# Optimization experiments

Measured on AMD Instinct MI355X. Metric: run time of the kernel, lower is better.

## Reference

```python
import jax, jax.numpy as jnp
import numpy as np

N, E, G = 50000, 800000, 512
F_IN, ED, NUM_CLASSES = 128, 3, 10
H1, C1, C2 = 4, 32, 64


def _add_self_loops(src, dst, eattr, n):
    # PyG add_self_loops with fill_value='mean': loop attr = mean of incoming edge attrs
    cnt = jax.ops.segment_sum(jnp.ones_like(dst, dtype=eattr.dtype), dst, num_segments=n)
    loop = jax.ops.segment_sum(eattr, dst, num_segments=n) / jnp.maximum(cnt, 1.0)[:, None]
    ar = jnp.arange(n)
    return (jnp.concatenate([src, ar]), jnp.concatenate([dst, ar]),
            jnp.concatenate([eattr, loop], axis=0))


def _gatv2(x, src, dst, eattr, Wl, bl, Wr, br, We, att, bias, heads, out_ch, concat, n):
    xl = (x @ Wl.T + bl).reshape(n, heads, out_ch)   # source transform (lin_l)
    xr = (x @ Wr.T + br).reshape(n, heads, out_ch)   # target transform (lin_r)
    ee = (eattr @ We.T).reshape(-1, heads, out_ch)   # edge transform (lin_edge, no bias)
    m = jax.nn.leaky_relu(xl[src] + xr[dst] + ee, 0.2)  # [E', H, C]
    score = jnp.einsum('ehc,hc->eh', m, att)
    # segment softmax over incoming edges of each target node
    smax = jax.ops.segment_max(score, dst, num_segments=n)
    ex = jnp.exp(score - smax[dst])
    denom = jax.ops.segment_sum(ex, dst, num_segments=n)
    alpha = ex / denom[dst]
    out = jax.ops.segment_sum(alpha[:, :, None] * xl[src], dst, num_segments=n)
    out = out.reshape(n, heads * out_ch) if concat else out.mean(axis=1)
    return out + bias


def setup_inputs() -> dict:
    key = jax.random.key(0)
    ks = jax.random.split(key, 24)
    s = 0.1
    return {
        'x': jax.random.normal(ks[0], (N, F_IN), jnp.float32),
        'edge_index': jax.random.randint(ks[1], (2, E), 0, N),
        'edge_attr': jax.random.normal(ks[2], (E, ED), jnp.float32),
        'batch': jnp.sort(jax.random.randint(ks[3], (N,), 0, G)),
        'u': jax.random.normal(ks[4], (G, 1), jnp.float32),
        'Wl1': jax.random.normal(ks[5], (H1 * C1, F_IN), jnp.float32) * s,
        'bl1': jnp.zeros((H1 * C1,), jnp.float32),
        'Wr1': jax.random.normal(ks[6], (H1 * C1, F_IN), jnp.float32) * s,
        'br1': jnp.zeros((H1 * C1,), jnp.float32),
        'We1': jax.random.normal(ks[7], (H1 * C1, ED), jnp.float32) * s,
        'att1': jax.random.normal(ks[8], (H1, C1), jnp.float32) * s,
        'b1': jnp.zeros((H1 * C1,), jnp.float32),
        'Wl2': jax.random.normal(ks[9], (C2, H1 * C1), jnp.float32) * s,
        'bl2': jnp.zeros((C2,), jnp.float32),
        'Wr2': jax.random.normal(ks[10], (C2, H1 * C1), jnp.float32) * s,
        'br2': jnp.zeros((C2,), jnp.float32),
        'We2': jax.random.normal(ks[11], (C2, ED), jnp.float32) * s,
        'att2': jax.random.normal(ks[12], (1, C2), jnp.float32) * s,
        'b2': jnp.zeros((C2,), jnp.float32),
        'W_lin1': jax.random.normal(ks[13], (32, 65), jnp.float32) * s,
        'b_lin1': jnp.zeros((32,), jnp.float32),
        'W_head': jax.random.normal(ks[14], (NUM_CLASSES, 32), jnp.float32) * s,
        'b_head': jnp.zeros((NUM_CLASSES,), jnp.float32),
    }


def reference(x, edge_index, edge_attr, batch, u,
              Wl1, bl1, Wr1, br1, We1, att1, b1,
              Wl2, bl2, Wr2, br2, We2, att2, b2,
              W_lin1, b_lin1, W_head, b_head):
    n = x.shape[0]
    src, dst, ea = _add_self_loops(edge_index[0], edge_index[1], edge_attr, n)
    h = jax.nn.elu(_gatv2(x, src, dst, ea, Wl1, bl1, Wr1, br1, We1, att1, b1, H1, C1, True, n))
    h = jax.nn.elu(_gatv2(h, src, dst, ea, Wl2, bl2, Wr2, br2, We2, att2, b2, 1, C2, False, n))
    cnt = jax.ops.segment_sum(jnp.ones((n,), h.dtype), batch, num_segments=G)
    pooled = jax.ops.segment_sum(h, batch, num_segments=G) / jnp.maximum(cnt, 1.0)[:, None]
    z = jax.nn.relu(jnp.concatenate([pooled, u], axis=1) @ W_lin1.T + b_lin1)
    return z @ W_head.T + b_head
```

## Files before the change

kernel.cpp:

```cpp
#include <hip/hip_runtime.h>
#include <hip/hip_fp16.h>
#include <math.h>


union H2U { __half2 h; unsigned u; };
typedef _Float16 hv2_t __attribute__((ext_vector_type(2)));
typedef unsigned uv4_t __attribute__((ext_vector_type(4)));
typedef _Float16 f16x8 __attribute__((ext_vector_type(8)));
typedef float f32x4 __attribute__((ext_vector_type(4)));

__device__ __forceinline__ __half2 hmax2(__half2 a, __half2 b) {
  union { __half2 h; hv2_t v; } x, y, r;
  x.h = a; y.h = b;
  r.v = __builtin_elementwise_max(x.v, y.v);
  return r.h;
}

#if __has_builtin(__builtin_amdgcn_fdot2)
__device__ __forceinline__ float dot2f(__half2 a, __half2 b, float c) {
  union { __half2 h; hv2_t v; } x, y;
  x.h = a; y.h = b;
  return __builtin_amdgcn_fdot2(x.v, y.v, c, false);
}
#else
__device__ __forceinline__ float dot2f(__half2 a, __half2 b, float c) {
  float2 af = __half22float2(a), bf = __half22float2(b);
  return fmaf(af.x, bf.x, fmaf(af.y, bf.y, c));
}
#endif

#if __has_builtin(__builtin_amdgcn_exp2f)
__device__ __forceinline__ float fexp2(float x) { return __builtin_amdgcn_exp2f(x); }
#else
__device__ __forceinline__ float fexp2(float x) { return exp2f(x); }
#endif

#if __has_builtin(__builtin_amdgcn_update_dpp)
template <int CTRL>
__device__ __forceinline__ float dpp_add(float v) {
  int r = __builtin_amdgcn_update_dpp(0, __builtin_bit_cast(int, v),
                                      CTRL, 0xf, 0xf, true);
  return v + __builtin_bit_cast(float, r);
}
__device__ __forceinline__ float row_sum16(float v) {
  v = dpp_add<0x121>(v);
  v = dpp_add<0x122>(v);
  v = dpp_add<0x124>(v);
  v = dpp_add<0x128>(v);
  return v;
}
#else
__device__ __forceinline__ float row_sum16(float v) {
  v += __shfl_xor(v, 1);
  v += __shfl_xor(v, 2);
  v += __shfl_xor(v, 4);
  v += __shfl_xor(v, 8);
  return v;
}
#endif

__device__ __forceinline__ float lowf(unsigned u) {
  H2U t; t.u = u;
  return __half2float(__low2half(t.h));
}

__device__ __forceinline__ float eluf(float x) {
  return x > 0.f ? x : __expf(x) - 1.0f;
}

__device__ __forceinline__ f16x8 cvt8(const float* __restrict__ p) {
  float4 v0 = *(const float4*)p;
  float4 v1 = *(const float4*)(p + 4);
  H2U h0, h1, h2, h3;
  h0.h = __floats2half2_rn(v0.x, v0.y);
  h1.h = __floats2half2_rn(v0.z, v0.w);
  h2.h = __floats2half2_rn(v1.x, v1.y);
  h3.h = __floats2half2_rn(v1.z, v1.w);
  union { uv4_t u; f16x8 v; } r;
  r.u = (uv4_t){h0.u, h1.u, h2.u, h3.u};
  return r.v;
}

#define LOG2E 1.44269504088896f

__global__ void hist_k(const int* __restrict__ dst, int* __restrict__ deg,
                       int* __restrict__ rank, int E) {
  int e = blockIdx.x * 256 + threadIdx.x;
  if (e < E) rank[e] = atomicAdd(&deg[dst[e]], 1);
}

__global__ void blocksum_k(const int* __restrict__ deg, int* __restrict__ bsum, int N) {
  __shared__ int s[256];
  int i = blockIdx.x * 256 + threadIdx.x;
  s[threadIdx.x] = (i < N) ? deg[i] : 0;
  __syncthreads();
  for (int off = 128; off; off >>= 1) {
    if (threadIdx.x < off) s[threadIdx.x] += s[threadIdx.x + off];
    __syncthreads();
  }
  if (threadIdx.x == 0) bsum[blockIdx.x] = s[0];
}

__global__ void writeptr_k(const int* __restrict__ deg, const int* __restrict__ bsum,
                           int* __restrict__ rowptr, int N, int E) {
  __shared__ int s[256];
  __shared__ int bs[256];
  int t = threadIdx.x;
  int i = blockIdx.x * 256 + t;
  bs[t] = (t < (int)blockIdx.x) ? bsum[t] : 0;
  s[t] = (i < N) ? deg[i] : 0;
  __syncthreads();
  for (int off = 128; off; off >>= 1) {
    if (t < off) bs[t] += bs[t + off];
    __syncthreads();
  }
  int base = bs[0];
  __syncthreads();
  for (int off = 1; off < 256; off <<= 1) {
    int v = (t >= off) ? s[t - off] : 0;
    __syncthreads();
    if (t >= off) s[t] += v;
    __syncthreads();
  }
  int excl = base + ((t == 0) ? 0 : s[t - 1]) + i;
  if (i < N) rowptr[i] = excl;
  if (i == N - 1) rowptr[N] = E + N;
}

__global__ void fill_k(const int* __restrict__ src, const int* __restrict__ dst,
                       const float* __restrict__ eattr, const int* __restrict__ rowptr,
                       const int* __restrict__ rank, uint4* __restrict__ erec, int E) {
  int e = blockIdx.x * 256 + threadIdx.x;
  if (e >= E) return;
  int pos = rowptr[dst[e]] + rank[e];
  H2U a0, a1, a2;
  float e0 = eattr[e * 3 + 0], e1 = eattr[e * 3 + 1], e2 = eattr[e * 3 + 2];
  a0.h = __floats2half2_rn(e0, e0);
  a1.h = __floats2half2_rn(e1, e1);
  a2.h = __floats2half2_rn(e2, e2);
  uv4_t v = {(unsigned)src[e], a0.u, a1.u, a2.u};
  __builtin_nontemporal_store(v, (uv4_t*)&erec[pos]);
}

__global__ void loopattr_k(const int* __restrict__ rowptr, uint4* __restrict__ erec, int N) {
  int lane = threadIdx.x & 63;
  int n = (int)((blockIdx.x * 256 + threadIdx.x) >> 6);
  if (n >= N) return;
  int beg = rowptr[n], endr = rowptr[n + 1] - 1;
  float f0 = 0.f, f1 = 0.f, f2 = 0.f;
  for (int i = beg + lane; i < endr; i += 64) {
    uint4 r = erec[i];
    f0 += lowf(r.y);
    f1 += lowf(r.z);
    f2 += lowf(r.w);
  }
#pragma unroll
  for (int off = 1; off < 64; off <<= 1) {
    f0 += __shfl_xor(f0, off);
    f1 += __shfl_xor(f1, off);
    f2 += __shfl_xor(f2, off);
  }
  if (lane == 0) {
    float inv = 1.0f / fmaxf((float)(endr - beg), 1.0f);
    H2U a0, a1, a2;
    a0.h = __floats2half2_rn(f0 * inv, f0 * inv);
    a1.h = __floats2half2_rn(f1 * inv, f1 * inv);
    a2.h = __floats2half2_rn(f2 * inv, f2 * inv);
    erec[endr] = make_uint4((unsigned)n, a0.u, a1.u, a2.u);
  }
}

__global__ void cvt_w_all_k(const float* __restrict__ Wl1, const float* __restrict__ Wr1,
                            const float* __restrict__ Wl2, const float* __restrict__ Wr2,
                            __half* __restrict__ wh1, __half* __restrict__ wh2) {
  int i = blockIdx.x * 256 + threadIdx.x;
  if (i >= 6144) return;
  const float* s;
  __half* d;
  int off;
  if (i < 2048)      { s = Wl1; d = wh1;         off = i; }
  else if (i < 4096) { s = Wr1; d = wh1 + 16384; off = i - 2048; }
  else if (i < 5120) { s = Wl2; d = wh2;         off = i - 4096; }
  else               { s = Wr2; d = wh2 + 8192;  off = i - 5120; }
  const float4* sp = (const float4*)(s + (size_t)off * 8);
  float4 v0 = sp[0], v1 = sp[1];
  H2U h0, h1, h2, h3;
  h0.h = __floats2half2_rn(v0.x, v0.y);
  h1.h = __floats2half2_rn(v0.z, v0.w);
  h2.h = __floats2half2_rn(v1.x, v1.y);
  h3.h = __floats2half2_rn(v1.z, v1.w);
  uv4_t o = {h0.u, h1.u, h2.u, h3.u};
  *(uv4_t*)(d + (size_t)off * 8) = o;
}

template <int J, bool F32IN>
__global__ __launch_bounds__(256) void mfma_linear2_k(
    const void* __restrict__ Xin, const __half* __restrict__ Wh,
    const float* __restrict__ b1v, const float* __restrict__ b2v,
    __half* __restrict__ out1, __half* __restrict__ out2, int N) {
  constexpr int CG = (2 * J) / 64;
  int lane = threadIdx.x & 63;
  int wid = __builtin_amdgcn_readfirstlane(
      (int)((blockIdx.x * 256 + threadIdx.x) >> 6));
  int rt = wid / CG;
  int cg = wid - rt * CG;
  int r0 = rt * 32;
  if (r0 >= N) return;

  int koff = (lane >> 4) * 8;
  int row0 = r0 + (lane & 15);
  int row1 = row0 + 16;
  int cr0 = min(row0, N - 1), cr1 = min(row1, N - 1);

  f16x8 a0[4], a1[4];
  if (F32IN) {
    const float* Xf = (const float*)Xin;
    const float* xp0 = Xf + (size_t)cr0 * 128 + koff;
    const float* xp1 = Xf + (size_t)cr1 * 128 + koff;
#pragma unroll
    for (int ks = 0; ks < 4; ++ks) {
      a0[ks] = cvt8(xp0 + ks * 32);
      a1[ks] = cvt8(xp1 + ks * 32);
    }
  } else {
    const __half* Xh = (const __half*)Xin;
    const __half* xp0 = Xh + (size_t)cr0 * 128 + koff;
    const __half* xp1 = Xh + (size_t)cr1 * 128 + koff;
#pragma unroll
    for (int ks = 0; ks < 4; ++ks) {
      a0[ks] = *(const f16x8*)(xp0 + ks * 32);
      a1[ks] = *(const f16x8*)(xp1 + ks * 32);
    }
  }

  bool isT1 = (cg * 64) < J;
  const float* bt = isT1 ? b1v : b2v;
  __half* op = isT1 ? out1 : out2;
  int cbase = cg * 64 - (isT1 ? 0 : J);
  int cl = cbase + (lane & 15);
  int rA = r0 + ((lane >> 4) << 2);

#pragma unroll
  for (int ct = 0; ct < 4; ++ct) {
    int col = cg * 64 + ct * 16 + (lane & 15);
    const __half* wp = Wh + (size_t)col * 128 + koff;
    f16x8 b0 = *(const f16x8*)(wp);
    f16x8 b1_ = *(const f16x8*)(wp + 32);
    f16x8 b2_ = *(const f16x8*)(wp + 64);
    f16x8 b3_ = *(const f16x8*)(wp + 96);
    f32x4 acc0 = {0.f, 0.f, 0.f, 0.f};
    f32x4 acc1 = {0.f, 0.f, 0.f, 0.f};
    acc0 = __builtin_amdgcn_mfma_f32_16x16x32_f16(a0[0], b0, acc0, 0, 0, 0);
    acc1 = __builtin_amdgcn_mfma_f32_16x16x32_f16(a1[0], b0, acc1, 0, 0, 0);
    acc0 = __builtin_amdgcn_mfma_f32_16x16x32_f16(a0[1], b1_, acc0, 0, 0, 0);
    acc1 = __builtin_amdgcn_mfma_f32_16x16x32_f16(a1[1], b1_, acc1, 0, 0, 0);
    acc0 = __builtin_amdgcn_mfma_f32_16x16x32_f16(a0[2], b2_, acc0, 0, 0, 0);
    acc1 = __builtin_amdgcn_mfma_f32_16x16x32_f16(a1[2], b2_, acc1, 0, 0, 0);
    acc0 = __builtin_amdgcn_mfma_f32_16x16x32_f16(a0[3], b3_, acc0, 0, 0, 0);
    acc1 = __builtin_amdgcn_mfma_f32_16x16x32_f16(a1[3], b3_, acc1, 0, 0, 0);

    int cc = cl + ct * 16;
    float bb = bt[cc];
#pragma unroll
    for (int q = 0; q < 4; ++q) {
      int r = rA + q;
      if (r < N) op[(size_t)r * J + cc] = __float2half(acc0[q] + bb);
      int r2 = r + 16;
      if (r2 < N) op[(size_t)r2 * J + cc] = __float2half(acc1[q] + bb);
    }
  }
}

__global__ __launch_bounds__(128) void gat1_fused_k(
    const int* __restrict__ rowptr, const uint4* __restrict__ erec,
    const __half* __restrict__ xlh, const __half* __restrict__ xrh,
    const float* __restrict__ We, const float* __restrict__ att,
    const float* __restrict__ bias, __half* __restrict__ out, int N) {
  constexpr int CH = 8;
  int lane = threadIdx.x & 63;
  int wave0 = __builtin_amdgcn_readfirstlane(
      (int)((blockIdx.x * blockDim.x + threadIdx.x) >> 6));
  int nwaves = (gridDim.x * blockDim.x) >> 6;
  const __half2* xl2p = (const __half2*)xlh;
  const __half2* xr2p = (const __half2*)xrh;
  __half2* outp = (__half2*)out;
  int c0 = 2 * lane;
  __half2 w0p = __floats2half2_rn(We[c0 * 3 + 0], We[c0 * 3 + 3]);
  __half2 w1p = __floats2half2_rn(We[c0 * 3 + 1], We[c0 * 3 + 4]);
  __half2 w2p = __floats2half2_rn(We[c0 * 3 + 2], We[c0 * 3 + 5]);
  __half2 attp = __floats2half2_rn(att[c0] * LOG2E, att[c0 + 1] * LOG2E);
  __half2 k02 = __floats2half2_rn(0.2f, 0.2f);
  float2 bv = make_float2(bias[c0], bias[c0 + 1]);

  for (int n = wave0; n < N; n += nwaves) {
    __half2 xrp = xr2p[(size_t)n * 64 + lane];
    int beg = rowptr[n], end = rowptr[n + 1];
    int cnt = end - beg;

    float acc0 = 0.f, acc1 = 0.f, den = 0.f;

    auto edge1 = [&](const uint4& rec, __half2 rf) {
      H2U e0, e1, e2;
      e0.u = rec.y; e1.u = rec.z; e2.u = rec.w;
      __half2 m = __hadd2(rf, xrp);
      m = __hfma2(e0.h, w0p, m);
      m = __hfma2(e1.h, w1p, m);
      m = __hfma2(e2.h, w2p, m);
      m = hmax2(m, __hmul2(m, k02));
      float v = row_sum16(dot2f(m, attp, 0.f));
      float ex = fexp2(v);
      float2 rfF = __half22float2(rf);
      den += ex;
      acc0 = fmaf(ex, rfF.x, acc0);
      acc1 = fmaf(ex, rfF.y, acc1);
    };

    int nfull = cnt / CH;
    for (int ch = 0; ch < nfull; ++ch) {
      int b = beg + ch * CH;
      uint4 recs[CH];
#pragma unroll
      for (int j = 0; j < CH; ++j) recs[j] = erec[b + j];
      __half2 r_[CH];
#pragma unroll
      for (int j = 0; j < CH; ++j) {
        int s = __builtin_amdgcn_readfirstlane((int)recs[j].x);
        r_[j] = xl2p[(size_t)s * 64 + lane];
      }
#pragma unroll
      for (int j = 0; j < CH; ++j) edge1(recs[j], r_[j]);
    }
    int gi = beg + nfull * CH;
    if (gi + 4 <= end) {
      uint4 recs[4];
#pragma unroll
      for (int j = 0; j < 4; ++j) recs[j] = erec[gi + j];
      __half2 r_[4];
#pragma unroll
      for (int j = 0; j < 4; ++j) {
        int s = __builtin_amdgcn_readfirstlane((int)recs[j].x);
        r_[j] = xl2p[(size_t)s * 64 + lane];
      }
#pragma unroll
      for (int j = 0; j < 4; ++j) edge1(recs[j], r_[j]);
      gi += 4;
    }
    for (; gi + 2 <= end; gi += 2) {
      uint4 recA = erec[gi];
      uint4 recB = erec[gi + 1];
      int sA = __builtin_amdgcn_readfirstlane((int)recA.x);
      int sB = __builtin_amdgcn_readfirstlane((int)recB.x);
      __half2 rfA = xl2p[(size_t)sA * 64 + lane];
      __half2 rfB = xl2p[(size_t)sB * 64 + lane];
      edge1(recA, rfA);
      edge1(recB, rfB);
    }
    if (gi < end) {
      uint4 rec = erec[gi];
      int s = __builtin_amdgcn_readfirstlane((int)rec.x);
      __half2 rf = xl2p[(size_t)s * 64 + lane];
      edge1(rec, rf);
    }

    float o0 = acc0 / den + bv.x;
    float o1 = acc1 / den + bv.y;
    o0 = o0 > 0.f ? o0 : __expf(o0) - 1.0f;
    o1 = o1 > 0.f ? o1 : __expf(o1) - 1.0f;
    H2U o;
    o.h = __floats2half2_rn(o0, o1);
    outp[(size_t)n * 64 + lane] = o.h;
  }
}

__global__ __launch_bounds__(128) void gat2_fused_k(
    const int* __restrict__ rowptr, const uint4* __restrict__ erec,
    const __half* __restrict__ xlh, const __half* __restrict__ xrh,
    const float* __restrict__ We, const float* __restrict__ att,
    const float* __restrict__ bias, float* __restrict__ out, int N) {
  int lane = threadIdx.x & 63;
  int s16 = lane & 15, qr = lane >> 4;
  int wave0 = __builtin_amdgcn_readfirstlane(
      (int)((blockIdx.x * blockDim.x + threadIdx.x) >> 6));
  int nwaves = (gridDim.x * blockDim.x) >> 6;
  int c4 = s16 * 4;

  __half2 w0A = __floats2half2_rn(We[(c4 + 0) * 3 + 0], We[(c4 + 1) * 3 + 0]);
  __half2 w0B = __floats2half2_rn(We[(c4 + 2) * 3 + 0], We[(c4 + 3) * 3 + 0]);
  __half2 w1A = __floats2half2_rn(We[(c4 + 0) * 3 + 1], We[(c4 + 1) * 3 + 1]);
  __half2 w1B = __floats2half2_rn(We[(c4 + 2) * 3 + 1], We[(c4 + 3) * 3 + 1]);
  __half2 w2A = __floats2half2_rn(We[(c4 + 0) * 3 + 2], We[(c4 + 1) * 3 + 2]);
  __half2 w2B = __floats2half2_rn(We[(c4 + 2) * 3 + 2], We[(c4 + 3) * 3 + 2]);
  __half2 attA = __floats2half2_rn(att[c4 + 0] * LOG2E, att[c4 + 1] * LOG2E);
  __half2 attB = __floats2half2_rn(att[c4 + 2] * LOG2E, att[c4 + 3] * LOG2E);
  __half2 k02 = __floats2half2_rn(0.2f, 0.2f);
  float4 bvv = make_float4(bias[c4], bias[c4 + 1], bias[c4 + 2], bias[c4 + 3]);

  for (int n = wave0; n < N; n += nwaves) {
    uint2 xu = *(const uint2*)&xrh[(size_t)n * 64 + c4];
    H2U xrA, xrB;
    xrA.u = xu.x; xrB.u = xu.y;
    int beg = rowptr[n], end = rowptr[n + 1];
    int cnt = end - beg;
    float a0 = 0.f, a1 = 0.f, a2 = 0.f, a3 = 0.f, den = 0.f;

    auto edge4 = [&](const uint4& rec, uint2 gu, bool valid) {
      H2U e0, e1, e2, gA, gB;
      e0.u = rec.y; e1.u = rec.z; e2.u = rec.w;
      gA.u = gu.x; gB.u = gu.y;
      __half2 tA = __hfma2(e2.h, w2A, xrA.h);
      tA = __hfma2(e1.h, w1A, tA);
      tA = __hfma2(e0.h, w0A, tA);
      __half2 mA = __hadd2(gA.h, tA);
      mA = hmax2(mA, __hmul2(mA, k02));
      __half2 tB = __hfma2(e2.h, w2B, xrB.h);
      tB = __hfma2(e1.h, w1B, tB);
      tB = __hfma2(e0.h, w0B, tB);
      __half2 mB = __hadd2(gB.h, tB);
      mB = hmax2(mB, __hmul2(mB, k02));
      float v = dot2f(mB, attB, dot2f(mA, attA, 0.f));
      v = row_sum16(v);
      float ex = valid ? fexp2(v) : 0.f;
      float2 fA = __half22float2(gA.h), fB = __half22float2(gB.h);
      den += ex;
      a0 = fmaf(ex, fA.x, a0);
      a1 = fmaf(ex, fA.y, a1);
      a2 = fmaf(ex, fB.x, a2);
      a3 = fmaf(ex, fB.y, a3);
    };

    int nch = cnt >> 3;
    for (int ch = 0; ch < nch; ++ch) {
      int b = beg + ch * 8 + qr;
      uint4 rec[2];
      uint2 gu[2];
#pragma unroll
      for (int j = 0; j < 2; ++j) rec[j] = erec[b + 4 * j];
#pragma unroll
      for (int j = 0; j < 2; ++j)
        gu[j] = *(const uint2*)(xlh + (size_t)rec[j].x * 64 + c4);
#pragma unroll
      for (int j = 0; j < 2; ++j) edge4(rec[j], gu[j], true);
    }
    for (int gi = beg + nch * 8; gi < end; gi += 4) {
      int idx = gi + qr;
      bool valid = idx < end;
      uint4 rec = erec[valid ? idx : (end - 1)];
      uint2 gu = *(const uint2*)(xlh + (size_t)rec.x * 64 + c4);
      edge4(rec, gu, valid);
    }

    a0 += __shfl_xor(a0, 16); a0 += __shfl_xor(a0, 32);
    a1 += __shfl_xor(a1, 16); a1 += __shfl_xor(a1, 32);
    a2 += __shfl_xor(a2, 16); a2 += __shfl_xor(a2, 32);
    a3 += __shfl_xor(a3, 16); a3 += __shfl_xor(a3, 32);
    den += __shfl_xor(den, 16); den += __shfl_xor(den, 32);

    if (lane < 16) {
      float4 o;
      o.x = eluf(a0 / den + bvv.x);
      o.y = eluf(a1 / den + bvv.y);
      o.z = eluf(a2 / den + bvv.z);
      o.w = eluf(a3 / den + bvv.w);
      *(float4*)&out[(size_t)n * 64 + c4] = o;
    }
  }
}

__global__ void final_mlp_k(const float* __restrict__ h2, const int* __restrict__ batch,
                            int N, const float* __restrict__ u,
                            const float* __restrict__ W1, const float* __restrict__ b1,
                            const float* __restrict__ Wh, const float* __restrict__ bh,
                            float* __restrict__ out) {
  __shared__ float comb[4][64];
  __shared__ float feat[65];
  __shared__ float z[32];
  int g = blockIdx.x;
  int t = threadIdx.x;
  int c = t & 63, q = t >> 6;
  int lo, hi;
  {
    int l = 0, h = N;
    while (l < h) { int m = (l + h) >> 1; if (batch[m] < g) l = m + 1; else h = m; }
    lo = l;
    h = N;
    while (l < h) { int m = (l + h) >> 1; if (batch[m] < g + 1) l = m + 1; else h = m; }
    hi = l;
  }
  float a = 0.f;
  for (int nn = lo + q; nn < hi; nn += 4) a += h2[(size_t)nn * 64 + c];
  comb[q][c] = a;
  __syncthreads();
  if (t < 64) {
    float s = comb[0][t] + comb[1][t] + comb[2][t] + comb[3][t];
    float inv = 1.0f / fmaxf((float)(hi - lo), 1.0f);
    feat[t] = s * inv;
    if (t == 0) feat[64] = u[g];
  }
  __syncthreads();
  if (t < 32) {
    float s = b1[t];
    for (int k = 0; k < 65; ++k) s += feat[k] * W1[t * 65 + k];
    z[t] = fmaxf(s, 0.0f);
  }
  __syncthreads();
  if (t < 10) {
    float s = bh[t];
    for (int k = 0; k < 32; ++k) s += z[k] * Wh[t * 32 + k];
    out[g * 10 + t] = s;
  }
}

extern "C" void kernel_launch(void* const* d_in, const int* in_sizes, int n_in,
                              void* d_out, int out_size, void* d_ws, size_t ws_size,
                              hipStream_t stream) {
  const float* x      = (const float*)d_in[0];
  const int*   eidx   = (const int*)d_in[1];
  const float* eattr  = (const float*)d_in[2];
  const int*   batch  = (const int*)d_in[3];
  const float* u      = (const float*)d_in[4];
  const float* Wl1    = (const float*)d_in[5];
  const float* bl1    = (const float*)d_in[6];
  const float* Wr1    = (const float*)d_in[7];
  const float* br1    = (const float*)d_in[8];
  const float* We1    = (const float*)d_in[9];
  const float* att1   = (const float*)d_in[10];
  const float* b1     = (const float*)d_in[11];
  const float* Wl2    = (const float*)d_in[12];
  const float* bl2    = (const float*)d_in[13];
  const float* Wr2    = (const float*)d_in[14];
  const float* br2    = (const float*)d_in[15];
  const float* We2    = (const float*)d_in[16];
  const float* att2   = (const float*)d_in[17];
  const float* b2     = (const float*)d_in[18];
  const float* W_lin1 = (const float*)d_in[19];
  const float* b_lin1 = (const float*)d_in[20];
  const float* W_head = (const float*)d_in[21];
  const float* b_head = (const float*)d_in[22];

  const int N = in_sizes[0] / 128;
  const int E = in_sizes[1] / 2;
  const int G = in_sizes[4];
  const int* srcp = eidx;
  const int* dstp = eidx + E;

  __half* bufh = (__half*)d_ws;
  __half* bufr = bufh + (size_t)N * 128;
  float* buf3 = (float*)(bufr + (size_t)N * 128);
  __half* g1h = (__half*)buf3;
  float* h2f = (float*)(g1h + (size_t)N * 128);
  uint4* erec = (uint4*)(buf3 + (size_t)N * 128);
  int* rank   = (int*)(erec + ((size_t)E + N));
  int* deg    = rank + E;
  int* rowptr = deg + N;
  int* bsum   = rowptr + N + 1;
  uintptr_t wtop = ((uintptr_t)(bsum + 256) + 15) & ~(uintptr_t)15;
  __half* wh1 = (__half*)wtop;
  __half* wh2 = wh1 + 32768;

  const int nb = (N + 255) / 256;
  const int gat_blocks = (N + 1) / 2;
  const int rt = (N + 31) / 32;

  cvt_w_all_k<<<24, 256, 0, stream>>>(Wl1, Wr1, Wl2, Wr2, wh1, wh2);
  mfma_linear2_k<128, true><<<rt, 256, 0, stream>>>(x, wh1, bl1, br1,
                                                    bufh, bufr, N);

  (void)hipMemsetAsync(deg, 0, sizeof(int) * (size_t)N, stream);
  hist_k<<<(E + 255) / 256, 256, 0, stream>>>(dstp, deg, rank, E);
  blocksum_k<<<nb, 256, 0, stream>>>(deg, bsum, N);
  writeptr_k<<<nb, 256, 0, stream>>>(deg, bsum, rowptr, N, E);
  fill_k<<<(E + 255) / 256, 256, 0, stream>>>(srcp, dstp, eattr, rowptr, rank, erec, E);
  loopattr_k<<<(N * 64 + 255) / 256, 256, 0, stream>>>(rowptr, erec, N);

  gat1_fused_k<<<gat_blocks, 128, 0, stream>>>(rowptr, erec, bufh, bufr,
                                               We1, att1, b1, g1h, N);

  mfma_linear2_k<64, false><<<(rt * 2 + 3) / 4, 256, 0, stream>>>(g1h, wh2,
                                                                  bl2, br2,
                                                                  bufh, bufr, N);
  gat2_fused_k<<<gat_blocks, 128, 0, stream>>>(rowptr, erec, bufh, bufr,
                                               We2, att2, b2, h2f, N);

  final_mlp_k<<<G, 256, 0, stream>>>(h2f, batch, N, u, W_lin1, b_lin1, W_head, b_head,
                                     (float*)d_out);
}
```

Before: 334.2 us.

## Replace rank array with atomic cursor fill and convert weights in-kernel

The CSR build no longer stores a per-edge rank from the histogram pass. The fill kernel instead claims slots by atomically incrementing a per-node cursor that is initialised from rowptr, which removes an E-sized write and read. The separate weight-conversion kernel is also dropped, so the MFMA linear kernel reads fp32 weights and converts them to fp16 in registers, saving one launch but redoing the conversion in every wave. The order of edges within each destination segment becomes nondeterministic, and the nontemporal store of edge records is replaced by a plain store.

```diff
diff --git a/kernel.cpp b/kernel.cpp
--- a/kernel.cpp
+++ b/kernel.cpp
@@ -83,10 +83,9 @@
 
 #define LOG2E 1.44269504088896f
 
-__global__ void hist_k(const int* __restrict__ dst, int* __restrict__ deg,
-                       int* __restrict__ rank, int E) {
+__global__ void hist_k(const int* __restrict__ dst, int* __restrict__ deg, int E) {
   int e = blockIdx.x * 256 + threadIdx.x;
-  if (e < E) rank[e] = atomicAdd(&deg[dst[e]], 1);
+  if (e < E) atomicAdd(&deg[dst[e]], 1);
 }
 
 __global__ void blocksum_k(const int* __restrict__ deg, int* __restrict__ bsum, int N) {
@@ -102,7 +101,8 @@
 }
 
 __global__ void writeptr_k(const int* __restrict__ deg, const int* __restrict__ bsum,
-                           int* __restrict__ rowptr, int N, int E) {
+                           int* __restrict__ rowptr, int* __restrict__ cursor,
+                           int N, int E) {
   __shared__ int s[256];
   __shared__ int bs[256];
   int t = threadIdx.x;
@@ -123,23 +123,26 @@
     __syncthreads();
   }
   int excl = base + ((t == 0) ? 0 : s[t - 1]) + i;
-  if (i < N) rowptr[i] = excl;
+  if (i < N) {
+    rowptr[i] = excl;
+    cursor[i] = excl;
+  }
   if (i == N - 1) rowptr[N] = E + N;
 }
 
 __global__ void fill_k(const int* __restrict__ src, const int* __restrict__ dst,
-                       const float* __restrict__ eattr, const int* __restrict__ rowptr,
-                       const int* __restrict__ rank, uint4* __restrict__ erec, int E) {
+                       const float* __restrict__ eattr, int* __restrict__ cursor,
+                       uint4* __restrict__ erec, int E) {
   int e = blockIdx.x * 256 + threadIdx.x;
   if (e >= E) return;
-  int pos = rowptr[dst[e]] + rank[e];
+  int d = dst[e];
+  int pos = atomicAdd(&cursor[d], 1);
   H2U a0, a1, a2;
   float e0 = eattr[e * 3 + 0], e1 = eattr[e * 3 + 1], e2 = eattr[e * 3 + 2];
   a0.h = __floats2half2_rn(e0, e0);
   a1.h = __floats2half2_rn(e1, e1);
   a2.h = __floats2half2_rn(e2, e2);
-  uv4_t v = {(unsigned)src[e], a0.u, a1.u, a2.u};
-  __builtin_nontemporal_store(v, (uv4_t*)&erec[pos]);
+  erec[pos] = make_uint4((unsigned)src[e], a0.u, a1.u, a2.u);
 }
 
 __global__ void loopattr_k(const int* __restrict__ rowptr, uint4* __restrict__ erec, int N) {
@@ -170,32 +173,10 @@
   }
 }
 
-__global__ void cvt_w_all_k(const float* __restrict__ Wl1, const float* __restrict__ Wr1,
-                            const float* __restrict__ Wl2, const float* __restrict__ Wr2,
-                            __half* __restrict__ wh1, __half* __restrict__ wh2) {
-  int i = blockIdx.x * 256 + threadIdx.x;
-  if (i >= 6144) return;
-  const float* s;
-  __half* d;
-  int off;
-  if (i < 2048)      { s = Wl1; d = wh1;         off = i; }
-  else if (i < 4096) { s = Wr1; d = wh1 + 16384; off = i - 2048; }
-  else if (i < 5120) { s = Wl2; d = wh2;         off = i - 4096; }
-  else               { s = Wr2; d = wh2 + 8192;  off = i - 5120; }
-  const float4* sp = (const float4*)(s + (size_t)off * 8);
-  float4 v0 = sp[0], v1 = sp[1];
-  H2U h0, h1, h2, h3;
-  h0.h = __floats2half2_rn(v0.x, v0.y);
-  h1.h = __floats2half2_rn(v0.z, v0.w);
-  h2.h = __floats2half2_rn(v1.x, v1.y);
-  h3.h = __floats2half2_rn(v1.z, v1.w);
-  uv4_t o = {h0.u, h1.u, h2.u, h3.u};
-  *(uv4_t*)(d + (size_t)off * 8) = o;
-}
-
 template <int J, bool F32IN>
 __global__ __launch_bounds__(256) void mfma_linear2_k(
-    const void* __restrict__ Xin, const __half* __restrict__ Wh,
+    const void* __restrict__ Xin,
+    const float* __restrict__ W1f, const float* __restrict__ W2f,
     const float* __restrict__ b1v, const float* __restrict__ b2v,
     __half* __restrict__ out1, __half* __restrict__ out2, int N) {
   constexpr int CG = (2 * J) / 64;
@@ -235,6 +216,7 @@
 
   bool isT1 = (cg * 64) < J;
   const float* bt = isT1 ? b1v : b2v;
+  const float* wt = isT1 ? W1f : W2f;
   __half* op = isT1 ? out1 : out2;
   int cbase = cg * 64 - (isT1 ? 0 : J);
   int cl = cbase + (lane & 15);
@@ -242,12 +224,12 @@
 
 #pragma unroll
   for (int ct = 0; ct < 4; ++ct) {
-    int col = cg * 64 + ct * 16 + (lane & 15);
-    const __half* wp = Wh + (size_t)col * 128 + koff;
-    f16x8 b0 = *(const f16x8*)(wp);
-    f16x8 b1_ = *(const f16x8*)(wp + 32);
-    f16x8 b2_ = *(const f16x8*)(wp + 64);
-    f16x8 b3_ = *(const f16x8*)(wp + 96);
+    int col = cbase + ct * 16 + (lane & 15);
+    const float* wp = wt + (size_t)col * 128 + koff;
+    f16x8 b0 = cvt8(wp);
+    f16x8 b1_ = cvt8(wp + 32);
+    f16x8 b2_ = cvt8(wp + 64);
+    f16x8 b3_ = cvt8(wp + 96);
     f32x4 acc0 = {0.f, 0.f, 0.f, 0.f};
     f32x4 acc1 = {0.f, 0.f, 0.f, 0.f};
     acc0 = __builtin_amdgcn_mfma_f32_16x16x32_f16(a0[0], b0, acc0, 0, 0, 0);
@@ -549,33 +531,29 @@
   __half* g1h = (__half*)buf3;
   float* h2f = (float*)(g1h + (size_t)N * 128);
   uint4* erec = (uint4*)(buf3 + (size_t)N * 128);
-  int* rank   = (int*)(erec + ((size_t)E + N));
-  int* deg    = rank + E;
+  int* cursor = (int*)(erec + ((size_t)E + N));
+  int* deg    = cursor + N;
   int* rowptr = deg + N;
   int* bsum   = rowptr + N + 1;
-  uintptr_t wtop = ((uintptr_t)(bsum + 256) + 15) & ~(uintptr_t)15;
-  __half* wh1 = (__half*)wtop;
-  __half* wh2 = wh1 + 32768;
 
   const int nb = (N + 255) / 256;
   const int gat_blocks = (N + 1) / 2;
   const int rt = (N + 31) / 32;
 
-  cvt_w_all_k<<<24, 256, 0, stream>>>(Wl1, Wr1, Wl2, Wr2, wh1, wh2);
-  mfma_linear2_k<128, true><<<rt, 256, 0, stream>>>(x, wh1, bl1, br1,
+  mfma_linear2_k<128, true><<<rt, 256, 0, stream>>>(x, Wl1, Wr1, bl1, br1,
                                                     bufh, bufr, N);
 
   (void)hipMemsetAsync(deg, 0, sizeof(int) * (size_t)N, stream);
-  hist_k<<<(E + 255) / 256, 256, 0, stream>>>(dstp, deg, rank, E);
+  hist_k<<<(E + 255) / 256, 256, 0, stream>>>(dstp, deg, E);
   blocksum_k<<<nb, 256, 0, stream>>>(deg, bsum, N);
-  writeptr_k<<<nb, 256, 0, stream>>>(deg, bsum, rowptr, N, E);
-  fill_k<<<(E + 255) / 256, 256, 0, stream>>>(srcp, dstp, eattr, rowptr, rank, erec, E);
+  writeptr_k<<<nb, 256, 0, stream>>>(deg, bsum, rowptr, cursor, N, E);
+  fill_k<<<(E + 255) / 256, 256, 0, stream>>>(srcp, dstp, eattr, cursor, erec, E);
   loopattr_k<<<(N * 64 + 255) / 256, 256, 0, stream>>>(rowptr, erec, N);
 
   gat1_fused_k<<<gat_blocks, 128, 0, stream>>>(rowptr, erec, bufh, bufr,
                                                We1, att1, b1, g1h, N);
 
-  mfma_linear2_k<64, false><<<(rt * 2 + 3) / 4, 256, 0, stream>>>(g1h, wh2,
+  mfma_linear2_k<64, false><<<(rt * 2 + 3) / 4, 256, 0, stream>>>(g1h, Wl2, Wr2,
                                                                   bl2, br2,
                                                                   bufh, bufr, N);
   gat2_fused_k<<<gat_blocks, 128, 0, stream>>>(rowptr, erec, bufh, bufr,
```

Result: slower. 369.1 us (+10.5%).

## Split each node's edges across two waves in gat1 and merge through LDS

Applied to the files above, without the earlier changes.

The first GAT aggregation kernel now assigns two waves to each target node instead of one. The waves take alternating 8-edge chunks, and the tail edges go to whichever wave would naturally take the next chunk. Partial numerators and denominators are combined through shared memory after a block barrier. This is meant to raise memory-level parallelism and latency hiding for the gathers at roughly 17 edges per node, at the cost of twice as many waves, an LDS reduction and a synchronisation per block.

```diff
diff --git a/kernel.cpp b/kernel.cpp
--- a/kernel.cpp
+++ b/kernel.cpp
@@ -271,16 +271,21 @@
   }
 }
 
-__global__ __launch_bounds__(128) void gat1_fused_k(
+__global__ __launch_bounds__(256) void gat1_fused_k(
     const int* __restrict__ rowptr, const uint4* __restrict__ erec,
     const __half* __restrict__ xlh, const __half* __restrict__ xrh,
     const float* __restrict__ We, const float* __restrict__ att,
     const float* __restrict__ bias, __half* __restrict__ out, int N) {
   constexpr int CH = 8;
-  int lane = threadIdx.x & 63;
-  int wave0 = __builtin_amdgcn_readfirstlane(
-      (int)((blockIdx.x * blockDim.x + threadIdx.x) >> 6));
-  int nwaves = (gridDim.x * blockDim.x) >> 6;
+  int tid = threadIdx.x;
+  int lane = tid & 63;
+  int w = (tid >> 6) & 1;
+  int pair = tid >> 7;
+  int n = blockIdx.x * 2 + pair;
+  bool active = n < N;
+
+  __shared__ float s0[2][64], s1[2][64], sden[2][64];
+
   const __half2* xl2p = (const __half2*)xlh;
   const __half2* xr2p = (const __half2*)xrh;
   __half2* outp = (__half2*)out;
@@ -292,31 +297,35 @@
   __half2 k02 = __floats2half2_rn(0.2f, 0.2f);
   float2 bv = make_float2(bias[c0], bias[c0 + 1]);
 
-  for (int n = wave0; n < N; n += nwaves) {
-    __half2 xrp = xr2p[(size_t)n * 64 + lane];
-    int beg = rowptr[n], end = rowptr[n + 1];
-    int cnt = end - beg;
-
-    float acc0 = 0.f, acc1 = 0.f, den = 0.f;
-
-    auto edge1 = [&](const uint4& rec, __half2 rf) {
-      H2U e0, e1, e2;
-      e0.u = rec.y; e1.u = rec.z; e2.u = rec.w;
-      __half2 m = __hadd2(rf, xrp);
-      m = __hfma2(e0.h, w0p, m);
-      m = __hfma2(e1.h, w1p, m);
-      m = __hfma2(e2.h, w2p, m);
-      m = hmax2(m, __hmul2(m, k02));
-      float v = row_sum16(dot2f(m, attp, 0.f));
-      float ex = fexp2(v);
-      float2 rfF = __half22float2(rf);
-      den += ex;
-      acc0 = fmaf(ex, rfF.x, acc0);
-      acc1 = fmaf(ex, rfF.y, acc1);
-    };
-
-    int nfull = cnt / CH;
-    for (int ch = 0; ch < nfull; ++ch) {
+  float acc0 = 0.f, acc1 = 0.f, den = 0.f;
+  __half2 xrp = __floats2half2_rn(0.f, 0.f);
+  int beg = 0, end = 0, nfull = 0;
+
+  if (active) {
+    xrp = xr2p[(size_t)n * 64 + lane];
+    beg = rowptr[n];
+    end = rowptr[n + 1];
+    nfull = (end - beg) / CH;
+  }
+
+  auto edge1 = [&](const uint4& rec, __half2 rf) {
+    H2U e0, e1, e2;
+    e0.u = rec.y; e1.u = rec.z; e2.u = rec.w;
+    __half2 m = __hadd2(rf, xrp);
+    m = __hfma2(e0.h, w0p, m);
+    m = __hfma2(e1.h, w1p, m);
+    m = __hfma2(e2.h, w2p, m);
+    m = hmax2(m, __hmul2(m, k02));
+    float v = row_sum16(dot2f(m, attp, 0.f));
+    float ex = fexp2(v);
+    float2 rfF = __half22float2(rf);
+    den += ex;
+    acc0 = fmaf(ex, rfF.x, acc0);
+    acc1 = fmaf(ex, rfF.y, acc1);
+  };
+
+  if (active) {
+    for (int ch = w; ch < nfull; ch += 2) {
       int b = beg + ch * CH;
       uint4 recs[CH];
 #pragma unroll
@@ -330,38 +339,51 @@
 #pragma unroll
       for (int j = 0; j < CH; ++j) edge1(recs[j], r_[j]);
     }
-    int gi = beg + nfull * CH;
-    if (gi + 4 <= end) {
-      uint4 recs[4];
-#pragma unroll
-      for (int j = 0; j < 4; ++j) recs[j] = erec[gi + j];
-      __half2 r_[4];
-#pragma unroll
-      for (int j = 0; j < 4; ++j) {
-        int s = __builtin_amdgcn_readfirstlane((int)recs[j].x);
-        r_[j] = xl2p[(size_t)s * 64 + lane];
+    if (w == (nfull & 1)) {
+      int gi = beg + nfull * CH;
+      if (gi + 4 <= end) {
+        uint4 recs[4];
+#pragma unroll
+        for (int j = 0; j < 4; ++j) recs[j] = erec[gi + j];
+        __half2 r_[4];
+#pragma unroll
+        for (int j = 0; j < 4; ++j) {
+          int s = __builtin_amdgcn_readfirstlane((int)recs[j].x);
+          r_[j] = xl2p[(size_t)s * 64 + lane];
+        }
+#pragma unroll
+        for (int j = 0; j < 4; ++j) edge1(recs[j], r_[j]);
+        gi += 4;
       }
-#pragma unroll
-      for (int j = 0; j < 4; ++j) edge1(recs[j], r_[j]);
-      gi += 4;
-    }
-    for (; gi + 2 <= end; gi += 2) {
-      uint4 recA = erec[gi];
-      uint4 recB = erec[gi + 1];
-      int sA = __builtin_amdgcn_readfirstlane((int)recA.x);
-      int sB = __builtin_amdgcn_readfirstlane((int)recB.x);
-      __half2 rfA = xl2p[(size_t)sA * 64 + lane];
-      __half2 rfB = xl2p[(size_t)sB * 64 + lane];
-      edge1(recA, rfA);
-      edge1(recB, rfB);
-    }
-    if (gi < end) {
-      uint4 rec = erec[gi];
-      int s = __builtin_amdgcn_readfirstlane((int)rec.x);
-      __half2 rf = xl2p[(size_t)s * 64 + lane];
-      edge1(rec, rf);
-    }
-
+      for (; gi + 2 <= end; gi += 2) {
+        uint4 recA = erec[gi];
+        uint4 recB = erec[gi + 1];
+        int sA = __builtin_amdgcn_readfirstlane((int)recA.x);
+        int sB = __builtin_amdgcn_readfirstlane((int)recB.x);
+        __half2 rfA = xl2p[(size_t)sA * 64 + lane];
+        __half2 rfB = xl2p[(size_t)sB * 64 + lane];
+        edge1(recA, rfA);
+        edge1(recB, rfB);
+      }
+      if (gi < end) {
+        uint4 rec = erec[gi];
+        int s = __builtin_amdgcn_readfirstlane((int)rec.x);
+        __half2 rf = xl2p[(size_t)s * 64 + lane];
+        edge1(rec, rf);
+      }
+    }
+  }
+
+  if (w == 1) {
+    s0[pair][lane] = acc0;
+    s1[pair][lane] = acc1;
+    sden[pair][lane] = den;
+  }
+  __syncthreads();
+  if (active && w == 0) {
+    acc0 += s0[pair][lane];
+    acc1 += s1[pair][lane];
+    den += sden[pair][lane];
     float o0 = acc0 / den + bv.x;
     float o1 = acc1 / den + bv.y;
     o0 = o0 > 0.f ? o0 : __expf(o0) - 1.0f;
@@ -572,8 +594,8 @@
   fill_k<<<(E + 255) / 256, 256, 0, stream>>>(srcp, dstp, eattr, rowptr, rank, erec, E);
   loopattr_k<<<(N * 64 + 255) / 256, 256, 0, stream>>>(rowptr, erec, N);
 
-  gat1_fused_k<<<gat_blocks, 128, 0, stream>>>(rowptr, erec, bufh, bufr,
-                                               We1, att1, b1, g1h, N);
+  gat1_fused_k<<<(N + 1) / 2, 256, 0, stream>>>(rowptr, erec, bufh, bufr,
+                                                We1, att1, b1, g1h, N);
 
   mfma_linear2_k<64, false><<<(rt * 2 + 3) / 4, 256, 0, stream>>>(g1h, wh2,
                                                                   bl2, br2,
```

Result: slower. 362.6 us (+8.5%).
